# Kernel optimization log

Hardware: AMD Instinct MI355X
Metric: run time of the kernel (lower is better)

Reference implementation:

```python
import jax, jax.numpy as jnp
import numpy as np
import math

N = 65536
IN_FEATURES = 64
OUT_FEATURES = 64
N_MODES = 32
N_BASIS = 1 + 2 * N_MODES


def setup_inputs() -> dict:
    key = jax.random.key(0)
    k1, k2 = jax.random.split(key)
    x = jax.random.normal(k1, (N, IN_FEATURES), dtype=jnp.float32)
    coeffs = jax.random.normal(k2, (OUT_FEATURES, IN_FEATURES, N_BASIS), dtype=jnp.float32) * 0.1
    bias = jnp.zeros((OUT_FEATURES,), dtype=jnp.float32)
    return {"x": x, "coeffs": coeffs, "bias": bias}


def reference(x, coeffs, bias):
    # freqs: [modes] = (1..modes) * pi
    freqs = jnp.arange(1, N_MODES + 1, dtype=x.dtype) * jnp.asarray(math.pi, dtype=x.dtype)
    x_flat = x.reshape(-1, IN_FEATURES)                      # [n, i]
    angles = x_flat[..., None] * freqs                       # [n, i, m]
    ones = jnp.ones(x_flat.shape + (1,), dtype=x.dtype)      # [n, i, 1]
    basis = jnp.concatenate([ones, jnp.sin(angles), jnp.cos(angles)], axis=-1)  # [n, i, b]
    out = jnp.einsum('oib,nib->no', coeffs, basis) + bias    # [n, o]
    return out.reshape(*x.shape[:-1], OUT_FEATURES)
```

## Files before the change

### kernel.cpp

```cpp
#include <hip/hip_runtime.h>
#include <hip/hip_bf16.h>


typedef __bf16 bf16x8 __attribute__((ext_vector_type(8)));
typedef float  f32x2  __attribute__((ext_vector_type(2)));
typedef float  f32x4  __attribute__((ext_vector_type(4)));
typedef float  f32x16 __attribute__((ext_vector_type(16)));

#define PI_F 3.14159265358979323846f

__global__ __launch_bounds__(256) void fkan_repack(
    const float* __restrict__ coeffs, const float* __restrict__ bias,
    __bf16* __restrict__ Bp, float* __restrict__ bias2) {
  int gid  = blockIdx.x * 256 + threadIdx.x;
  int lane = gid & 63;
  int frag = gid >> 6;
  int m  = frag >> 4;
  int kc = (frag >> 1) & 7;
  int cc = frag & 1;
  int o  = cc * 32 + (lane & 31);
  int kq = lane >> 5;

  bf16x8 v;
  #pragma unroll
  for (int t = 0; t < 8; ++t) {
    int i = kc * 8 + kq * 4 + (t >> 1);
    int b = (t & 1) ? (33 + m) : (1 + m);
    v[t] = (__bf16)coeffs[(o * 64 + i) * 65 + b];
  }
  *(bf16x8*)(Bp + (size_t)frag * 512 + lane * 8) = v;

  if (blockIdx.x == 0 && threadIdx.x < 64) {
    int oo = threadIdx.x;
    float s = bias[oo];
    #pragma unroll 4
    for (int ii = 0; ii < 64; ++ii) s += coeffs[(oo * 64 + ii) * 65 + 0];
    bias2[oo] = s;
  }
}

__device__ __forceinline__ void stage_slice(const __bf16* __restrict__ Bp,
                                            __bf16* dst, int m, int wave,
                                            int lane) {
  const char* g = (const char*)Bp + (size_t)m * 16384 + wave * 4096 + lane * 16;
  char* l = (char*)dst + wave * 4096;
  #pragma unroll
  for (int r = 0; r < 4; ++r) {
    __builtin_amdgcn_global_load_lds(
        (const __attribute__((address_space(1))) void*)(g + r * 1024),
        (__attribute__((address_space(3))) void*)(l + r * 1024), 16, 0, 0);
  }
}

#define ASM_VMCNT(N) asm volatile("s_waitcnt vmcnt(" #N ")" ::: "memory")

__device__ __forceinline__ void block_barrier() {
  asm volatile("" ::: "memory");
  __builtin_amdgcn_s_barrier();
  asm volatile("" ::: "memory");
}

__device__ __forceinline__ void compute_mode(const __bf16* bsrc, int lane,
                                             const f32x2* cur, f32x2* nxt,
                                             const float* T, f32x16* acc) {
  #pragma unroll
  for (int kc = 0; kc < 8; ++kc) {
    bf16x8 af;
    #pragma unroll
    for (int e = 0; e < 4; ++e) {
      af[2 * e]     = (__bf16)cur[kc * 4 + e][0];
      af[2 * e + 1] = (__bf16)cur[kc * 4 + e][1];
    }
    #pragma unroll
    for (int c2 = 0; c2 < 2; ++c2) {
      bf16x8 bf = *(const bf16x8*)(bsrc + (kc * 2 + c2) * 512 + lane * 8);
      acc[c2] = __builtin_amdgcn_mfma_f32_32x32x16_bf16(af, bf, acc[c2],
                                                        0, 0, 0);
    }
  }
  #pragma unroll
  for (int p = 0; p < 32; ++p) {
    f32x2 n;
    n[0] = fmaf(T[p], cur[p][0], -nxt[p][0]);
    n[1] = fmaf(T[p], cur[p][1], -nxt[p][1]);
    nxt[p] = n;
  }
}

__global__ __launch_bounds__(256, 2) void fkan_main(
    const float* __restrict__ x, const __bf16* __restrict__ Bp,
    const float* __restrict__ bias2, float* __restrict__ out) {
  __shared__ __bf16 Bs[4][8192];

  int tid  = threadIdx.x;
  int wave = tid >> 6;
  int lane = tid & 63;
  int kq   = lane >> 5;
  int cl   = lane & 31;
  int row  = blockIdx.x * 128 + wave * 32 + cl;

  float T[32];
  f32x2 cur[32], prv[32];
  const float* xrow = x + (size_t)row * 64 + kq * 4;
  #pragma unroll
  for (int kc = 0; kc < 8; ++kc) {
    f32x4 v = *(const f32x4*)(xrow + kc * 8);
    #pragma unroll
    for (int e = 0; e < 4; ++e) {
      int p = kc * 4 + e;
      float ss, cs;
      __sincosf(PI_F * v[e], &ss, &cs);
      T[p] = 2.0f * cs;
      cur[p][0] = ss;  cur[p][1] = cs;
      prv[p][0] = 0.f; prv[p][1] = 1.f;
    }
  }

  f32x16 acc[2];
  #pragma unroll
  for (int c2 = 0; c2 < 2; ++c2)
    #pragma unroll
    for (int r = 0; r < 16; ++r) acc[c2][r] = 0.f;

  stage_slice(Bp, &Bs[0][0], 0, wave, lane);
  stage_slice(Bp, &Bs[1][0], 1, wave, lane);

  #pragma unroll 1
  for (int mm = 0; mm < 28; mm += 2) {
    stage_slice(Bp, &Bs[(mm + 2) & 3][0], mm + 2, wave, lane);
    ASM_VMCNT(8);
    block_barrier();
    compute_mode(&Bs[mm & 3][0], lane, cur, prv, T, acc);

    stage_slice(Bp, &Bs[(mm + 3) & 3][0], mm + 3, wave, lane);
    ASM_VMCNT(8);
    block_barrier();
    compute_mode(&Bs[(mm + 1) & 3][0], lane, prv, cur, T, acc);
  }

  stage_slice(Bp, &Bs[2][0], 30, wave, lane);
  ASM_VMCNT(8);  block_barrier();
  compute_mode(&Bs[0][0], lane, cur, prv, T, acc);

  stage_slice(Bp, &Bs[3][0], 31, wave, lane);
  ASM_VMCNT(8);  block_barrier();
  compute_mode(&Bs[1][0], lane, prv, cur, T, acc);

  ASM_VMCNT(4);  block_barrier();
  compute_mode(&Bs[2][0], lane, cur, prv, T, acc);

  ASM_VMCNT(0);  block_barrier();
  compute_mode(&Bs[3][0], lane, prv, cur, T, acc);

  float* orow = out + (size_t)(blockIdx.x * 128 + wave * 32) * 64;
  #pragma unroll
  for (int c2 = 0; c2 < 2; ++c2) {
    float b2 = bias2[c2 * 32 + cl];
    #pragma unroll
    for (int r = 0; r < 16; ++r) {
      int ro = (r & 3) + 8 * (r >> 2) + 4 * kq;
      orow[(size_t)ro * 64 + c2 * 32 + cl] = acc[c2][r] + b2;
    }
  }
}

extern "C" void kernel_launch(void* const* d_in, const int* in_sizes, int n_in,
                              void* d_out, int out_size, void* d_ws, size_t ws_size,
                              hipStream_t stream) {
  const float* x      = (const float*)d_in[0];
  const float* coeffs = (const float*)d_in[1];
  const float* bias   = (const float*)d_in[2];
  float* out = (float*)d_out;

  __bf16* Bp   = (__bf16*)d_ws;
  float* bias2 = (float*)((char*)d_ws + 512 * 1024);

  int n_rows = in_sizes[0] / 64;

  fkan_repack<<<128, 256, 0, stream>>>(coeffs, bias, Bp, bias2);
  fkan_main<<<n_rows / 128, 256, 0, stream>>>(x, Bp, bias2, out);
}
```

Before: 118.0 us.

## Hand-schedule LDS reads with inline asm and unroll mode loop by four

Replaces the compiler-generated LDS fragment loads with inline-asm ds_read_b128 calls that use immediate offsets. Manual lgkmcnt waits let MFMAs start while later fragments are still in flight. The mode loop is unrolled by four so the LDS buffer indices become compile-time constants. The sin/cos state is split into separate scalar arrays, and the memory clobbers around the barriers are removed. This aims to cut address arithmetic and hide LDS latency. Without the memory clobbers, reordering across barriers could become fragile.

```diff
diff --git a/kernel.cpp b/kernel.cpp
--- a/kernel.cpp
+++ b/kernel.cpp
@@ -3,7 +3,6 @@
 
 
 typedef __bf16 bf16x8 __attribute__((ext_vector_type(8)));
-typedef float  f32x2  __attribute__((ext_vector_type(2)));
 typedef float  f32x4  __attribute__((ext_vector_type(4)));
 typedef float  f32x16 __attribute__((ext_vector_type(16)));
 
@@ -52,38 +51,55 @@
   }
 }
 
-#define ASM_VMCNT(N) asm volatile("s_waitcnt vmcnt(" #N ")" ::: "memory")
-
-__device__ __forceinline__ void block_barrier() {
-  asm volatile("" ::: "memory");
-  __builtin_amdgcn_s_barrier();
-  asm volatile("" ::: "memory");
-}
-
-__device__ __forceinline__ void compute_mode(const __bf16* bsrc, int lane,
-                                             const f32x2* cur, f32x2* nxt,
-                                             const float* T, f32x16* acc) {
-  #pragma unroll
-  for (int kc = 0; kc < 8; ++kc) {
-    bf16x8 af;
-    #pragma unroll
-    for (int e = 0; e < 4; ++e) {
-      af[2 * e]     = (__bf16)cur[kc * 4 + e][0];
-      af[2 * e + 1] = (__bf16)cur[kc * 4 + e][1];
-    }
-    #pragma unroll
-    for (int c2 = 0; c2 < 2; ++c2) {
-      bf16x8 bf = *(const bf16x8*)(bsrc + (kc * 2 + c2) * 512 + lane * 8);
-      acc[c2] = __builtin_amdgcn_mfma_f32_32x32x16_bf16(af, bf, acc[c2],
-                                                        0, 0, 0);
-    }
-  }
+typedef __attribute__((address_space(3))) const char* lds_ptr_t;
+
+#define DSRD(d, b, OFF) \
+  asm volatile("ds_read_b128 %0, %1 offset:" #OFF : "=v"(d) : "v"(b))
+
+#define LGKMW(N, a, b) \
+  asm volatile("s_waitcnt lgkmcnt(" #N ")" : "+v"(a), "+v"(b))
+
+#define ASM_VMCNT(N) asm volatile("s_waitcnt vmcnt(" #N ")")
+
+__device__ __forceinline__ void mode_compute(lds_ptr_t base,
+    const float* sA, const float* cA, float* sN, float* cN,
+    const float* T, f32x16* acc) {
+  bf16x8 f00, f01, f10, f11, f20, f21, f30, f31;
+  bf16x8 f40, f41, f50, f51, f60, f61, f70, f71;
+
+  DSRD(f00, base, 0);     DSRD(f01, base, 1024);
+  DSRD(f10, base, 2048);  DSRD(f11, base, 3072);
+  DSRD(f20, base, 4096);  DSRD(f21, base, 5120);
+  DSRD(f30, base, 6144);  DSRD(f31, base, 7168);
+
+#define AF(kc) bf16x8 af##kc; {                                         \
+    af##kc[0] = (__bf16)sA[kc * 4 + 0]; af##kc[1] = (__bf16)cA[kc * 4 + 0]; \
+    af##kc[2] = (__bf16)sA[kc * 4 + 1]; af##kc[3] = (__bf16)cA[kc * 4 + 1]; \
+    af##kc[4] = (__bf16)sA[kc * 4 + 2]; af##kc[5] = (__bf16)cA[kc * 4 + 2]; \
+    af##kc[6] = (__bf16)sA[kc * 4 + 3]; af##kc[7] = (__bf16)cA[kc * 4 + 3]; }
+#define MM(kc, fa, fb)                                                        \
+    acc[0] = __builtin_amdgcn_mfma_f32_32x32x16_bf16(af##kc, fa, acc[0], 0, 0, 0); \
+    acc[1] = __builtin_amdgcn_mfma_f32_32x32x16_bf16(af##kc, fb, acc[1], 0, 0, 0);
+
+  DSRD(f40, base, 8192);  DSRD(f41, base, 9216);
+  AF(0); LGKMW(8, f00, f01); MM(0, f00, f01);
+  DSRD(f50, base, 10240); DSRD(f51, base, 11264);
+  AF(1); LGKMW(8, f10, f11); MM(1, f10, f11);
+  DSRD(f60, base, 12288); DSRD(f61, base, 13312);
+  AF(2); LGKMW(8, f20, f21); MM(2, f20, f21);
+  DSRD(f70, base, 14336); DSRD(f71, base, 15360);
+  AF(3); LGKMW(8, f30, f31); MM(3, f30, f31);
+  AF(4); LGKMW(6, f40, f41); MM(4, f40, f41);
+  AF(5); LGKMW(4, f50, f51); MM(5, f50, f51);
+  AF(6); LGKMW(2, f60, f61); MM(6, f60, f61);
+  AF(7); LGKMW(0, f70, f71); MM(7, f70, f71);
+#undef AF
+#undef MM
+
   #pragma unroll
   for (int p = 0; p < 32; ++p) {
-    f32x2 n;
-    n[0] = fmaf(T[p], cur[p][0], -nxt[p][0]);
-    n[1] = fmaf(T[p], cur[p][1], -nxt[p][1]);
-    nxt[p] = n;
+    sN[p] = fmaf(T[p], sA[p], -sN[p]);
+    cN[p] = fmaf(T[p], cA[p], -cN[p]);
   }
 }
 
@@ -99,8 +115,12 @@
   int cl   = lane & 31;
   int row  = blockIdx.x * 128 + wave * 32 + cl;
 
-  float T[32];
-  f32x2 cur[32], prv[32];
+  lds_ptr_t base0 = (lds_ptr_t)(&Bs[0][0]) + lane * 16;
+  lds_ptr_t base1 = base0 + 16384;
+  lds_ptr_t base2 = base0 + 32768;
+  lds_ptr_t base3 = base0 + 49152;
+
+  float T[32], sp[32], cp[32], sc[32], cc_[32];
   const float* xrow = x + (size_t)row * 64 + kq * 4;
   #pragma unroll
   for (int kc = 0; kc < 8; ++kc) {
@@ -111,8 +131,8 @@
       float ss, cs;
       __sincosf(PI_F * v[e], &ss, &cs);
       T[p] = 2.0f * cs;
-      cur[p][0] = ss;  cur[p][1] = cs;
-      prv[p][0] = 0.f; prv[p][1] = 1.f;
+      sc[p] = ss;  cc_[p] = cs;
+      sp[p] = 0.f; cp[p] = 1.f;
     }
   }
 
@@ -126,31 +146,45 @@
   stage_slice(Bp, &Bs[1][0], 1, wave, lane);
 
   #pragma unroll 1
-  for (int mm = 0; mm < 28; mm += 2) {
-    stage_slice(Bp, &Bs[(mm + 2) & 3][0], mm + 2, wave, lane);
-    ASM_VMCNT(8);
-    block_barrier();
-    compute_mode(&Bs[mm & 3][0], lane, cur, prv, T, acc);
-
-    stage_slice(Bp, &Bs[(mm + 3) & 3][0], mm + 3, wave, lane);
-    ASM_VMCNT(8);
-    block_barrier();
-    compute_mode(&Bs[(mm + 1) & 3][0], lane, prv, cur, T, acc);
+  for (int mm = 0; mm < 28; mm += 4) {
+    stage_slice(Bp, &Bs[2][0], mm + 2, wave, lane);
+    ASM_VMCNT(8);
+    __builtin_amdgcn_s_barrier();
+    mode_compute(base0, sc, cc_, sp, cp, T, acc);
+
+    stage_slice(Bp, &Bs[3][0], mm + 3, wave, lane);
+    ASM_VMCNT(8);
+    __builtin_amdgcn_s_barrier();
+    mode_compute(base1, sp, cp, sc, cc_, T, acc);
+
+    stage_slice(Bp, &Bs[0][0], mm + 4, wave, lane);
+    ASM_VMCNT(8);
+    __builtin_amdgcn_s_barrier();
+    mode_compute(base2, sc, cc_, sp, cp, T, acc);
+
+    stage_slice(Bp, &Bs[1][0], mm + 5, wave, lane);
+    ASM_VMCNT(8);
+    __builtin_amdgcn_s_barrier();
+    mode_compute(base3, sp, cp, sc, cc_, T, acc);
   }
 
   stage_slice(Bp, &Bs[2][0], 30, wave, lane);
-  ASM_VMCNT(8);  block_barrier();
-  compute_mode(&Bs[0][0], lane, cur, prv, T, acc);
+  ASM_VMCNT(8);
+  __builtin_amdgcn_s_barrier();
+  mode_compute(base0, sc, cc_, sp, cp, T, acc);
 
   stage_slice(Bp, &Bs[3][0], 31, wave, lane);
-  ASM_VMCNT(8);  block_barrier();
-  compute_mode(&Bs[1][0], lane, prv, cur, T, acc);
-
-  ASM_VMCNT(4);  block_barrier();
-  compute_mode(&Bs[2][0], lane, cur, prv, T, acc);
-
-  ASM_VMCNT(0);  block_barrier();
-  compute_mode(&Bs[3][0], lane, prv, cur, T, acc);
+  ASM_VMCNT(8);
+  __builtin_amdgcn_s_barrier();
+  mode_compute(base1, sp, cp, sc, cc_, T, acc);
+
+  ASM_VMCNT(4);
+  __builtin_amdgcn_s_barrier();
+  mode_compute(base2, sc, cc_, sp, cp, T, acc);
+
+  ASM_VMCNT(0);
+  __builtin_amdgcn_s_barrier();
+  mode_compute(base3, sp, cp, sc, cc_, T, acc);
 
   float* orow = out + (size_t)(blockIdx.x * 128 + wave * 32) * 64;
   #pragma unroll
```

After: 267.6 us. +126.7%, slower.
